# Performance work log

Measured on AMD Instinct MI355X. Metric: run time of the kernel, lower is better.

Reference implementation:

```python
import jax, jax.numpy as jnp
import numpy as np

D_MODEL = 1024
NUM_HEADS = 16
HEAD_DIM = D_MODEL // NUM_HEADS


def setup_inputs() -> dict:
    key = jax.random.key(0)
    ks = jax.random.split(key, 9)
    B, S = 2, 2048
    scale = 1.0 / np.sqrt(D_MODEL)
    inp = {
        "x": jax.random.normal(ks[0], (B, S, D_MODEL), dtype=jnp.float32),
        "Wq": jax.random.normal(ks[1], (D_MODEL, D_MODEL), dtype=jnp.float32) * scale,
        "bq": jnp.zeros((D_MODEL,), dtype=jnp.float32),
        "Wk": jax.random.normal(ks[2], (D_MODEL, D_MODEL), dtype=jnp.float32) * scale,
        "bk": jnp.zeros((D_MODEL,), dtype=jnp.float32),
        "Wv": jax.random.normal(ks[3], (D_MODEL, D_MODEL), dtype=jnp.float32) * scale,
        "bv": jnp.zeros((D_MODEL,), dtype=jnp.float32),
        "Wo": jax.random.normal(ks[4], (D_MODEL, D_MODEL), dtype=jnp.float32) * scale,
        "bo": jnpp_zeros(D_MODEL) if False else jnp.zeros((D_MODEL,), dtype=jnp.float32),
    }
    return inp


def reference(x, Wq, bq, Wk, bk, Wv, bv, Wo, bo):
    B, S, _ = x.shape
    # projections (torch Linear: y = x @ W.T + b; here W stored as [in, out])
    q = x @ Wq + bq  # [B,S,D]
    k = x @ Wk + bk
    v = x @ Wv + bv
    # split heads -> [B,H,S,hd]
    def split(t):
        return t.reshape(B, S, NUM_HEADS, HEAD_DIM).transpose(0, 2, 1, 3)
    q, k, v = split(q), split(k), split(v)
    scale = 1.0 / jnp.sqrt(jnp.asarray(HEAD_DIM, dtype=x.dtype))
    scores = jnp.einsum("bhqd,bhkd->bhqk", q, k) * scale  # [B,H,S,S]
    probs = jax.nn.softmax(scores, axis=-1)
    out = jnp.einsum("bhqk,bhkd->bhqd", probs, v)  # [B,H,S,hd]
    out = out.transpose(0, 2, 1, 3).reshape(B, S, D_MODEL)
    return out @ Wo + bo  # dropout is identity in eval mode
```

## Files before the change

kernel.cpp:

```cpp
#include <hip/hip_runtime.h>

#define D_MODEL 1024
#define NHEADS  16
#define HDIM    64
#define BATCH   2
#define SEQ     2048
#define M_TOK   (BATCH * SEQ)

typedef unsigned short u16;
typedef unsigned int   u32;
typedef __attribute__((ext_vector_type(8))) short  short8;
typedef __attribute__((ext_vector_type(4))) float  floatx4;
typedef __attribute__((ext_vector_type(2))) u32    u32x2;

#define GLOBAL_AS __attribute__((address_space(1)))
#define LDS_AS    __attribute__((address_space(3)))

static __device__ __forceinline__ void gload_lds16(const u16* g, u16* l) {
    __builtin_amdgcn_global_load_lds((const GLOBAL_AS u32*)g, (LDS_AS u32*)l, 16, 0, 0);
}

static __device__ __forceinline__ u16 f2bf(float f) {
    union { float f; u32 i; } v; v.f = f;
    u32 x = v.i;
    return (u16)((x + 0x7fffu + ((x >> 16) & 1u)) >> 16);
}

static __device__ __forceinline__ u32 cvtpk(float a, float b) {
    u32 r;
    asm("v_cvt_pk_bf16_f32 %0, %1, %2" : "=v"(r) : "v"(a), "v"(b));
    return r;
}

static __device__ __forceinline__ short8 ld8_cvt(const float* __restrict__ p) {
    float4 f0 = *(const float4*)(p);
    float4 f1 = *(const float4*)(p + 4);
    short8 r;
    r[0] = (short)f2bf(f0.x); r[1] = (short)f2bf(f0.y);
    r[2] = (short)f2bf(f0.z); r[3] = (short)f2bf(f0.w);
    r[4] = (short)f2bf(f1.x); r[5] = (short)f2bf(f1.y);
    r[6] = (short)f2bf(f1.z); r[7] = (short)f2bf(f1.w);
    return r;
}

__global__ __launch_bounds__(256) void zerofill_k(float* __restrict__ out, int n) {
    int i = blockIdx.x * 256 + threadIdx.x;
    if (i < n) out[i] = 0.f;
}

__global__ __launch_bounds__(256) void prep_k(const float* __restrict__ x,
                                              const float* __restrict__ W0,
                                              const float* __restrict__ W1,
                                              const float* __restrict__ W2,
                                              const float* __restrict__ W3,
                                              u16* __restrict__ WtBase,
                                              u16* __restrict__ Xb) {
    int z = blockIdx.z;
    int t = threadIdx.x;
    if (z == 4) {
        int blk = blockIdx.y * 32 + blockIdx.x;
        size_t i0 = ((size_t)blk * 256 + t) * 16;
        short8 v0 = ld8_cvt(x + i0);
        short8 v1 = ld8_cvt(x + i0 + 8);
        *(short8*)(Xb + i0)     = v0;
        *(short8*)(Xb + i0 + 8) = v1;
        return;
    }
    const float* W = (z == 0) ? W0 : (z == 1) ? W1 : (z == 2) ? W2 : W3;
    u16* Wt = WtBase + (size_t)z * 1024 * 1024;
    __shared__ u16 T[32][34];
    int bx = blockIdx.x * 32, by = blockIdx.y * 32;
    {
        int r = t >> 3, c4 = t & 7;
        float4 f = *(const float4*)(W + (size_t)(by + r) * 1024 + bx + c4 * 4);
        u32 lo = (u32)f2bf(f.x) | ((u32)f2bf(f.y) << 16);
        u32 hi = (u32)f2bf(f.z) | ((u32)f2bf(f.w) << 16);
        *(u32*)(&T[r][c4 * 4])     = lo;
        *(u32*)(&T[r][c4 * 4 + 2]) = hi;
    }
    __syncthreads();
    if (t < 128) {
        int n = t >> 2, seg = t & 3;
        short8 v;
#pragma unroll
        for (int i = 0; i < 8; ++i) v[i] = (short)T[seg * 8 + i][n];
        *(short8*)(Wt + (size_t)(bx + n) * 1024 + by + seg * 8) = v;
    }
}

template <int MODE, int OUTF32, int MI>
static __device__ __forceinline__ void gemm_core(u16* __restrict__ smem,
                                                 const u16* __restrict__ A,
                                                 const u16* __restrict__ Bt,
                                                 const float* __restrict__ bias,
                                                 float scale,
                                                 void* __restrict__ C,
                                                 int m0, int n0) {
    u16* As = smem;
    u16* Bs = smem + MI * 32 * 64;
    int tid  = threadIdx.x;
    int wave = tid >> 6, lane = tid & 63;
    int quad = lane >> 4, l15 = lane & 15;
    int wm = (wave & 1) * (MI * 16);
    int wn = (wave >> 1) * 64;

    floatx4 acc[MI][4] = {};

    for (int k0 = 0; k0 < 1024; k0 += 64) {
#pragma unroll
        for (int t = 0; t < MI; ++t) {
            int a = t * 256 + tid;
            int row = a >> 3, c = a & 7;
            gload_lds16(A + (size_t)(m0 + row) * 1024 + k0 + ((c ^ (row & 7)) * 8),
                        As + (size_t)a * 8);
        }
#pragma unroll
        for (int t = 0; t < 4; ++t) {
            int a = t * 256 + tid;
            int row = a >> 3, c = a & 7;
            gload_lds16(Bt + (size_t)(n0 + row) * 1024 + k0 + ((c ^ (row & 7)) * 8),
                        Bs + (size_t)a * 8);
        }
        __syncthreads();

#pragma unroll
        for (int h = 0; h < 2; ++h) {
            int g = ((h * 4 + quad) ^ (l15 & 7)) * 8;
            short8 af[MI], bfr[4];
#pragma unroll
            for (int i = 0; i < MI; ++i)
                af[i] = *(const short8*)(As + (wm + i * 16 + l15) * 64 + g);
#pragma unroll
            for (int j = 0; j < 4; ++j)
                bfr[j] = *(const short8*)(Bs + (wn + j * 16 + l15) * 64 + g);
#pragma unroll
            for (int i = 0; i < MI; ++i)
#pragma unroll
                for (int j = 0; j < 4; ++j)
                    acc[i][j] = __builtin_amdgcn_mfma_f32_16x16x32_bf16(af[i], bfr[j], acc[i][j], 0, 0, 0);
        }
        __syncthreads();
    }

    if constexpr (MODE == 2) {
        u16* T = smem;
        int bb = m0 >> 11;
#pragma unroll
        for (int p = 0; p < 2; ++p) {
            if (p) __syncthreads();
            if ((wave >> 1) == p) {
#pragma unroll
                for (int j = 0; j < 4; ++j) {
                    int dcol = j * 16 + l15;
                    float bv = bias[n0 + p * 64 + dcol];
#pragma unroll
                    for (int i = 0; i < MI; ++i) {
#pragma unroll
                        for (int rr = 0; rr < 2; ++rr) {
                            int srow = wm + i * 16 + quad * 4 + rr * 2;
                            u16 lo = f2bf((acc[i][j][rr * 2]     + bv) * scale);
                            u16 hi = f2bf((acc[i][j][rr * 2 + 1] + bv) * scale);
                            *(u32*)(T + dcol * 136 + srow) = (u32)lo | ((u32)hi << 16);
                        }
                    }
                }
            }
            __syncthreads();
            int d  = tid >> 2;
            int sc = (tid & 3) * 32;
            int col = n0 + p * 64 + d;
            int h = col >> 6, dd = col & 63;
            int s0 = (m0 & 2047) + sc;
            size_t gbase = (((size_t)bb * NHEADS + h) * HDIM + dd) * SEQ + s0;
#pragma unroll
            for (int c = 0; c < 4; ++c)
                *(short8*)((u16*)C + gbase + c * 8) = *(const short8*)(T + d * 136 + sc + c * 8);
        }
        return;
    }

#pragma unroll
    for (int j = 0; j < 4; ++j) {
        int col = n0 + wn + j * 16 + l15;
        float bv = bias[col];
#pragma unroll
        for (int i = 0; i < MI; ++i) {
#pragma unroll
            for (int r = 0; r < 4; ++r) {
                int row = m0 + wm + i * 16 + quad * 4 + r;
                float v = (acc[i][j][r] + bv) * scale;
                size_t idx;
                if (MODE == 0) {
                    idx = (size_t)row * 1024 + col;
                } else {
                    int b = row >> 11, s = row & 2047;
                    int h = col >> 6,  d = col & 63;
                    idx = (((size_t)b * NHEADS + h) * SEQ + s) * HDIM + d;
                }
                if constexpr (OUTF32) ((float*)C)[idx] = v;
                else                  ((u16*)C)[idx] = f2bf(v);
            }
        }
    }
}

__global__ __launch_bounds__(256, 3) void gemm_qkv(const u16* __restrict__ X,
                                                   const u16* __restrict__ WtBase,
                                                   const float* __restrict__ bq,
                                                   const float* __restrict__ bk,
                                                   const float* __restrict__ bv,
                                                   u16* __restrict__ OutBase) {
    __shared__ __align__(16) u16 smem[16384];
    int z = blockIdx.z;
    const u16* Bt     = WtBase + (size_t)z * 1024 * 1024;
    const float* bias = (z == 0) ? bq : (z == 1) ? bk : bv;
    u16* C            = OutBase + (size_t)z * (size_t)M_TOK * 1024;
    if (z == 2)
        gemm_core<2, 0, 4>(smem, X, Bt, bias, 1.0f, C, blockIdx.y * 128, blockIdx.x * 128);
    else if (z == 0)
        gemm_core<1, 0, 4>(smem, X, Bt, bias, 0.18033688011112042f , C,
                           blockIdx.y * 128, blockIdx.x * 128);
    else
        gemm_core<1, 0, 4>(smem, X, Bt, bias, 1.0f, C, blockIdx.y * 128, blockIdx.x * 128);
}

__global__ __launch_bounds__(256, 2) void gemm_out(const u16* __restrict__ A,
                                                   const u16* __restrict__ Bt,
                                                   const float* __restrict__ bias,
                                                   float* __restrict__ C) {
    __shared__ __align__(16) u16 smem[12288];
    gemm_core<0, 1, 2>(smem, A, Bt, bias, 1.0f, C, blockIdx.y * 64, blockIdx.x * 128);
}

#define PST2 40
__global__ __launch_bounds__(512, 3) void attn_k(const u16* __restrict__ Q,
                                                 const u16* __restrict__ K,
                                                 const u16* __restrict__ Vt_g,
                                                 u16* __restrict__ O) {
    __shared__ __align__(16) u16 Vt[2][64 * 128];
    __shared__ __align__(16) u16 Kt[2][128 * 64];
    __shared__ __align__(16) u16 Pl[8][16 * PST2];

    int tid  = threadIdx.x;
    int wave = tid >> 6, lane = tid & 63;
    int quad = lane >> 4, l15 = lane & 15;
    int bh = blockIdx.y;
    int b = bh >> 4, h = bh & 15;
    const u16* Qb = Q    + (size_t)bh * SEQ * HDIM;
    const u16* Kb = K    + (size_t)bh * SEQ * HDIM;
    const u16* Vb = Vt_g + (size_t)bh * HDIM * SEQ;
    int q0 = blockIdx.x * 128 + wave * 16;

    short8 qf0 = *(const short8*)(Qb + (size_t)(q0 + l15) * 64 + quad * 8);
    short8 qf1 = *(const short8*)(Qb + (size_t)(q0 + l15) * 64 + 32 + quad * 8);

    short8 onesf;
#pragma unroll
    for (int i = 0; i < 8; ++i) onesf[i] = (short)0x3F80;

    floatx4 o[4] = {};
    floatx4 o_sum = {};

    {
#pragma unroll
        for (int rnd = 0; rnd < 2; ++rnd) {
            int g = rnd * 512 + tid;
            int vrow = g >> 4, vc = g & 15;
            gload_lds16(Vb + (size_t)vrow * SEQ + (vc ^ (vrow & 15)) * 8,
                        Vt[0] + (size_t)g * 8);
            int krow = g >> 3, kc = g & 7;
            gload_lds16(Kb + (size_t)krow * 64 + (kc ^ (krow & 7)) * 8,
                        Kt[0] + (size_t)g * 8);
        }
    }

    for (int it = 0; it < SEQ / 128; ++it) {
        int kv0 = it * 128;
        __syncthreads();

        if (it + 1 < SEQ / 128) {
            u16* vdst = Vt[(it + 1) & 1];
            u16* kdst = Kt[(it + 1) & 1];
#pragma unroll
            for (int rnd = 0; rnd < 2; ++rnd) {
                int g = rnd * 512 + tid;
                int vrow = g >> 4, vc = g & 15;
                gload_lds16(Vb + (size_t)vrow * SEQ + kv0 + 128 + (vc ^ (vrow & 15)) * 8,
                            vdst + (size_t)g * 8);
                int krow = g >> 3, kc = g & 7;
                gload_lds16(Kb + (size_t)(kv0 + 128 + krow) * 64 + (kc ^ (krow & 7)) * 8,
                            kdst + (size_t)g * 8);
            }
        }

        const u16* kb = Kt[it & 1];
        floatx4 s[8];
        __builtin_amdgcn_s_setprio(1);
#pragma unroll
        for (int j = 0; j < 8; ++j) {
            int row = j * 16 + l15;
            const u16* kr = kb + (size_t)row * 64;
            short8 k0 = *(const short8*)(kr + ((quad ^ (l15 & 7)) * 8));
            short8 k1 = *(const short8*)(kr + (((quad + 4) ^ (l15 & 7)) * 8));
            floatx4 a = {};
            a = __builtin_amdgcn_mfma_f32_16x16x32_bf16(k0, qf0, a, 0, 0, 0);
            a = __builtin_amdgcn_mfma_f32_16x16x32_bf16(k1, qf1, a, 0, 0, 0);
            s[j] = a;
        }
        __builtin_amdgcn_s_setprio(0);

        const u16* vb = Vt[it & 1];
#pragma unroll
        for (int kh = 0; kh < 4; ++kh) {
#pragma unroll
            for (int t = 0; t < 2; ++t) {
                int j = kh * 2 + t;
                float p0 = exp2f(s[j][0]), p1 = exp2f(s[j][1]);
                float p2 = exp2f(s[j][2]), p3 = exp2f(s[j][3]);
                u32 w0 = cvtpk(p0, p1), w1 = cvtpk(p2, p3);
                *(u32x2*)(&Pl[wave][l15 * PST2 + t * 16 + quad * 4]) = (u32x2){w0, w1};
            }
            short8 pf = *(const short8*)(&Pl[wave][l15 * PST2 + quad * 8]);
            __builtin_amdgcn_s_setprio(1);
#pragma unroll
            for (int dj = 0; dj < 4; ++dj) {
                int row = dj * 16 + l15;
                int cg  = kh * 4 + quad;
                short8 vf = *(const short8*)(&vb[(row * 16 + (cg ^ l15)) * 8]);
                o[dj] = __builtin_amdgcn_mfma_f32_16x16x32_bf16(pf, vf, o[dj], 0, 0, 0);
            }
            o_sum = __builtin_amdgcn_mfma_f32_16x16x32_bf16(pf, onesf, o_sum, 0, 0, 0);
            __builtin_amdgcn_s_setprio(0);
        }
    }

#pragma unroll
    for (int r = 0; r < 4; ++r) {
        float invq = 1.f / o_sum[r];
        int srow = q0 + quad * 4 + r;
        size_t base = ((size_t)b * SEQ + srow) * D_MODEL + h * HDIM;
#pragma unroll
        for (int dj = 0; dj < 4; ++dj)
            O[base + dj * 16 + l15] = f2bf(o[dj][r] * invq);
    }
}

extern "C" void kernel_launch(void* const* d_in, const int* in_sizes, int n_in,
                              void* d_out, int out_size, void* d_ws, size_t ws_size,
                              hipStream_t stream) {
    const float* x  = (const float*)d_in[0];
    const float* Wq = (const float*)d_in[1];
    const float* bq = (const float*)d_in[2];
    const float* Wk = (const float*)d_in[3];
    const float* bk = (const float*)d_in[4];
    const float* Wv = (const float*)d_in[5];
    const float* bv = (const float*)d_in[6];
    const float* Wo = (const float*)d_in[7];
    const float* bo = (const float*)d_in[8];
    float* out = (float*)d_out;

    char* ws = (char*)d_ws;
    const size_t WSZ = (size_t)1024 * 1024 * sizeof(u16);
    const size_t QSZ = (size_t)M_TOK * 1024 * sizeof(u16);
    const size_t NEED = 4 * WSZ + 4 * QSZ;

    if (ws_size < NEED) {
        zerofill_k<<<dim3((out_size + 255) / 256), 256, 0, stream>>>(out, out_size);
        return;
    }

    u16* wtq = (u16*)(ws);
    u16* wto = (u16*)(ws + 3 * WSZ);
    u16* Qw  = (u16*)(ws + 4 * WSZ);
    u16* Kw  = (u16*)(ws + 4 * WSZ + QSZ);
    u16* Vw  = (u16*)(ws + 4 * WSZ + 2 * QSZ);
    u16* Xb  = (u16*)(ws + 4 * WSZ + 3 * QSZ);
    u16* Aw  = Xb;

    prep_k<<<dim3(32, 32, 5), 256, 0, stream>>>(x, Wq, Wk, Wv, Wo, wtq, Xb);

    gemm_qkv<<<dim3(8, 32, 3), 256, 0, stream>>>(Xb, wtq, bq, bk, bv, Qw);
    attn_k<<<dim3(SEQ / 128, BATCH * NHEADS), 512, 0, stream>>>(Qw, Kw, Vw, Aw);
    gemm_out<<<dim3(8, 64), 256, 0, stream>>>(Aw, wto, bo, out);
}
```

Baseline: 196.6 us.

## Double-buffer GEMM K-loop with async LDS prefetch and per-kernel BK

Adds a templated K-tile size and double-buffers the GEMM main loop. The next tile is now issued via global_load_lds before the current tile's MFMAs run, so there is one barrier per iteration instead of two. The QKV GEMM switches to BK=32 tiles with no XOR swizzle so the double buffer fits its existing shared-memory size. The output GEMM keeps BK=64 and doubles its shared allocation. This is meant to hide global load latency behind compute, at the cost of possible LDS bank conflicts in the unswizzled BK=32 layout and more shared memory in gemm_out.

```diff
diff --git a/kernel.cpp b/kernel.cpp
--- a/kernel.cpp
+++ b/kernel.cpp
@@ -88,7 +88,7 @@
     }
 }
 
-template <int MODE, int OUTF32, int MI>
+template <int MODE, int OUTF32, int MI, int BK>
 static __device__ __forceinline__ void gemm_core(u16* __restrict__ smem,
                                                  const u16* __restrict__ A,
                                                  const u16* __restrict__ Bt,
@@ -96,53 +96,70 @@
                                                  float scale,
                                                  void* __restrict__ C,
                                                  int m0, int n0) {
-    u16* As = smem;
-    u16* Bs = smem + MI * 32 * 64;
+    constexpr int RG   = BK / 8;
+    constexpr int BUFG = (MI * 32 + 128) * RG;
     int tid  = threadIdx.x;
     int wave = tid >> 6, lane = tid & 63;
     int quad = lane >> 4, l15 = lane & 15;
     int wm = (wave & 1) * (MI * 16);
     int wn = (wave >> 1) * 64;
 
+    auto stage = [&](int buf, int k0) {
+        u16* Asb = smem + (size_t)buf * BUFG * 8;
+        u16* Bsb = Asb + MI * 32 * RG * 8;
+#pragma unroll
+        for (int t = 0; t < MI * 32 * RG / 256; ++t) {
+            int a = t * 256 + tid;
+            int row = a / RG, c = a & (RG - 1);
+            int cs = (BK == 64) ? (c ^ (row & 7)) : c;
+            gload_lds16(A + (size_t)(m0 + row) * 1024 + k0 + cs * 8,
+                        Asb + (size_t)a * 8);
+        }
+#pragma unroll
+        for (int t = 0; t < 128 * RG / 256; ++t) {
+            int a = t * 256 + tid;
+            int row = a / RG, c = a & (RG - 1);
+            int cs = (BK == 64) ? (c ^ (row & 7)) : c;
+            gload_lds16(Bt + (size_t)(n0 + row) * 1024 + k0 + cs * 8,
+                        Bsb + (size_t)a * 8);
+        }
+    };
+
     floatx4 acc[MI][4] = {};
-
-    for (int k0 = 0; k0 < 1024; k0 += 64) {
-#pragma unroll
-        for (int t = 0; t < MI; ++t) {
-            int a = t * 256 + tid;
-            int row = a >> 3, c = a & 7;
-            gload_lds16(A + (size_t)(m0 + row) * 1024 + k0 + ((c ^ (row & 7)) * 8),
-                        As + (size_t)a * 8);
-        }
-#pragma unroll
-        for (int t = 0; t < 4; ++t) {
-            int a = t * 256 + tid;
-            int row = a >> 3, c = a & 7;
-            gload_lds16(Bt + (size_t)(n0 + row) * 1024 + k0 + ((c ^ (row & 7)) * 8),
-                        Bs + (size_t)a * 8);
-        }
+    stage(0, 0);
+
+    for (int k0 = 0; k0 < 1024; k0 += BK) {
+        int cur = (k0 / BK) & 1;
         __syncthreads();
-
-#pragma unroll
-        for (int h = 0; h < 2; ++h) {
-            int g = ((h * 4 + quad) ^ (l15 & 7)) * 8;
+        if (k0 + BK < 1024) stage(cur ^ 1, k0 + BK);
+
+        u16* Asb = smem + (size_t)cur * BUFG * 8;
+        u16* Bsb = Asb + MI * 32 * RG * 8;
+#pragma unroll
+        for (int h = 0; h < BK / 32; ++h) {
             short8 af[MI], bfr[4];
 #pragma unroll
-            for (int i = 0; i < MI; ++i)
-                af[i] = *(const short8*)(As + (wm + i * 16 + l15) * 64 + g);
-#pragma unroll
-            for (int j = 0; j < 4; ++j)
-                bfr[j] = *(const short8*)(Bs + (wn + j * 16 + l15) * 64 + g);
+            for (int i = 0; i < MI; ++i) {
+                int row = wm + i * 16 + l15;
+                int g = (BK == 64) ? ((h * 4 + quad) ^ (l15 & 7)) : quad;
+                af[i] = *(const short8*)(Asb + (size_t)row * BK + g * 8);
+            }
+#pragma unroll
+            for (int j = 0; j < 4; ++j) {
+                int row = wn + j * 16 + l15;
+                int g = (BK == 64) ? ((h * 4 + quad) ^ (l15 & 7)) : quad;
+                bfr[j] = *(const short8*)(Bsb + (size_t)row * BK + g * 8);
+            }
 #pragma unroll
             for (int i = 0; i < MI; ++i)
 #pragma unroll
                 for (int j = 0; j < 4; ++j)
                     acc[i][j] = __builtin_amdgcn_mfma_f32_16x16x32_bf16(af[i], bfr[j], acc[i][j], 0, 0, 0);
         }
+    }
+
+    if constexpr (MODE == 2) {
         __syncthreads();
-    }
-
-    if constexpr (MODE == 2) {
         u16* T = smem;
         int bb = m0 >> 11;
 #pragma unroll
@@ -216,20 +233,20 @@
     const float* bias = (z == 0) ? bq : (z == 1) ? bk : bv;
     u16* C            = OutBase + (size_t)z * (size_t)M_TOK * 1024;
     if (z == 2)
-        gemm_core<2, 0, 4>(smem, X, Bt, bias, 1.0f, C, blockIdx.y * 128, blockIdx.x * 128);
+        gemm_core<2, 0, 4, 32>(smem, X, Bt, bias, 1.0f, C, blockIdx.y * 128, blockIdx.x * 128);
     else if (z == 0)
-        gemm_core<1, 0, 4>(smem, X, Bt, bias, 0.18033688011112042f , C,
-                           blockIdx.y * 128, blockIdx.x * 128);
+        gemm_core<1, 0, 4, 32>(smem, X, Bt, bias, 0.18033688011112042f , C,
+                               blockIdx.y * 128, blockIdx.x * 128);
     else
-        gemm_core<1, 0, 4>(smem, X, Bt, bias, 1.0f, C, blockIdx.y * 128, blockIdx.x * 128);
+        gemm_core<1, 0, 4, 32>(smem, X, Bt, bias, 1.0f, C, blockIdx.y * 128, blockIdx.x * 128);
 }
 
 __global__ __launch_bounds__(256, 2) void gemm_out(const u16* __restrict__ A,
                                                    const u16* __restrict__ Bt,
                                                    const float* __restrict__ bias,
                                                    float* __restrict__ C) {
-    __shared__ __align__(16) u16 smem[12288];
-    gemm_core<0, 1, 2>(smem, A, Bt, bias, 1.0f, C, blockIdx.y * 64, blockIdx.x * 128);
+    __shared__ __align__(16) u16 smem[24576];
+    gemm_core<0, 1, 2, 64>(smem, A, Bt, bias, 1.0f, C, blockIdx.y * 64, blockIdx.x * 128);
 }
 
 #define PST2 40
```

Measured after the change: 196.2 us. No clear change (-0.2%).

## Triple-buffer GEMM K-loop with async LDS loads and XCD-aware block remap

Applied to the files above, without the earlier changes.

Restructures the shared GEMM core so the K loop runs in 32-wide steps over three LDS buffers. Loads for step k+2 are issued before the MFMAs of step k, and explicit vmcnt waits plus a single barrier per step replace the two syncthreads per 64-wide step. It also drops the XOR swizzle, which may reintroduce LDS bank conflicts. The QKV and output GEMM grids remap block indices so that consecutive logical tiles land on the same XCD for L2 reuse. Larger LDS use may lower occupancy.

```diff
diff --git a/kernel.cpp b/kernel.cpp
--- a/kernel.cpp
+++ b/kernel.cpp
@@ -96,53 +96,64 @@
                                                  float scale,
                                                  void* __restrict__ C,
                                                  int m0, int n0) {
-    u16* As = smem;
-    u16* Bs = smem + MI * 32 * 64;
+    constexpr int BUFU = (MI * 32 + 128) * 32;
+    constexpr int NK   = 32;
     int tid  = threadIdx.x;
     int wave = tid >> 6, lane = tid & 63;
     int quad = lane >> 4, l15 = lane & 15;
     int wm = (wave & 1) * (MI * 16);
     int wn = (wave >> 1) * 64;
 
+    auto stage = [&](int buf, int k0) {
+        u16* Asb = smem + (size_t)buf * BUFU;
+        u16* Bsb = Asb + MI * 32 * 32;
+#pragma unroll
+        for (int t = 0; t < MI / 2; ++t) {
+            int a = t * 256 + tid;
+            gload_lds16(A + (size_t)(m0 + (a >> 2)) * 1024 + k0 + (a & 3) * 8,
+                        Asb + (size_t)a * 8);
+        }
+#pragma unroll
+        for (int t = 0; t < 2; ++t) {
+            int a = t * 256 + tid;
+            gload_lds16(Bt + (size_t)(n0 + (a >> 2)) * 1024 + k0 + (a & 3) * 8,
+                        Bsb + (size_t)a * 8);
+        }
+    };
+
     floatx4 acc[MI][4] = {};
-
-    for (int k0 = 0; k0 < 1024; k0 += 64) {
-#pragma unroll
-        for (int t = 0; t < MI; ++t) {
-            int a = t * 256 + tid;
-            int row = a >> 3, c = a & 7;
-            gload_lds16(A + (size_t)(m0 + row) * 1024 + k0 + ((c ^ (row & 7)) * 8),
-                        As + (size_t)a * 8);
-        }
-#pragma unroll
-        for (int t = 0; t < 4; ++t) {
-            int a = t * 256 + tid;
-            int row = a >> 3, c = a & 7;
-            gload_lds16(Bt + (size_t)(n0 + row) * 1024 + k0 + ((c ^ (row & 7)) * 8),
-                        Bs + (size_t)a * 8);
-        }
+    stage(0, 0);
+    stage(1, 32);
+
+    for (int k = 0; k < NK; ++k) {
+        if (k + 1 < NK) {
+            if constexpr (MI == 4) asm volatile("s_waitcnt vmcnt(4)" ::: "memory");
+            else                   asm volatile("s_waitcnt vmcnt(3)" ::: "memory");
+        } else {
+            asm volatile("s_waitcnt vmcnt(0)" ::: "memory");
+        }
+        __builtin_amdgcn_s_barrier();
+        __builtin_amdgcn_sched_barrier(0);
+        if (k + 2 < NK) stage((k + 2) % 3, (k + 2) * 32);
+
+        u16* Asb = smem + (size_t)(k % 3) * BUFU;
+        u16* Bsb = Asb + MI * 32 * 32;
+        short8 af[MI], bfr[4];
+#pragma unroll
+        for (int i = 0; i < MI; ++i)
+            af[i] = *(const short8*)(Asb + (wm + i * 16 + l15) * 32 + quad * 8);
+#pragma unroll
+        for (int j = 0; j < 4; ++j)
+            bfr[j] = *(const short8*)(Bsb + (wn + j * 16 + l15) * 32 + quad * 8);
+#pragma unroll
+        for (int i = 0; i < MI; ++i)
+#pragma unroll
+            for (int j = 0; j < 4; ++j)
+                acc[i][j] = __builtin_amdgcn_mfma_f32_16x16x32_bf16(af[i], bfr[j], acc[i][j], 0, 0, 0);
+    }
+
+    if constexpr (MODE == 2) {
         __syncthreads();
-
-#pragma unroll
-        for (int h = 0; h < 2; ++h) {
-            int g = ((h * 4 + quad) ^ (l15 & 7)) * 8;
-            short8 af[MI], bfr[4];
-#pragma unroll
-            for (int i = 0; i < MI; ++i)
-                af[i] = *(const short8*)(As + (wm + i * 16 + l15) * 64 + g);
-#pragma unroll
-            for (int j = 0; j < 4; ++j)
-                bfr[j] = *(const short8*)(Bs + (wn + j * 16 + l15) * 64 + g);
-#pragma unroll
-            for (int i = 0; i < MI; ++i)
-#pragma unroll
-                for (int j = 0; j < 4; ++j)
-                    acc[i][j] = __builtin_amdgcn_mfma_f32_16x16x32_bf16(af[i], bfr[j], acc[i][j], 0, 0, 0);
-        }
-        __syncthreads();
-    }
-
-    if constexpr (MODE == 2) {
         u16* T = smem;
         int bb = m0 >> 11;
 #pragma unroll
@@ -210,26 +221,32 @@
                                                    const float* __restrict__ bk,
                                                    const float* __restrict__ bv,
                                                    u16* __restrict__ OutBase) {
-    __shared__ __align__(16) u16 smem[16384];
-    int z = blockIdx.z;
+    __shared__ __align__(16) u16 smem[24576];
+    int hw = blockIdx.z * 256 + blockIdx.y * 8 + blockIdx.x;
+    int lg = (hw & 7) * 96 + (hw >> 3);
+    int z  = lg >> 8;
+    int rem = lg & 255;
+    int m0 = (rem >> 3) * 128, n0 = (rem & 7) * 128;
     const u16* Bt     = WtBase + (size_t)z * 1024 * 1024;
     const float* bias = (z == 0) ? bq : (z == 1) ? bk : bv;
     u16* C            = OutBase + (size_t)z * (size_t)M_TOK * 1024;
     if (z == 2)
-        gemm_core<2, 0, 4>(smem, X, Bt, bias, 1.0f, C, blockIdx.y * 128, blockIdx.x * 128);
+        gemm_core<2, 0, 4>(smem, X, Bt, bias, 1.0f, C, m0, n0);
     else if (z == 0)
-        gemm_core<1, 0, 4>(smem, X, Bt, bias, 0.18033688011112042f , C,
-                           blockIdx.y * 128, blockIdx.x * 128);
+        gemm_core<1, 0, 4>(smem, X, Bt, bias, 0.18033688011112042f , C, m0, n0);
     else
-        gemm_core<1, 0, 4>(smem, X, Bt, bias, 1.0f, C, blockIdx.y * 128, blockIdx.x * 128);
+        gemm_core<1, 0, 4>(smem, X, Bt, bias, 1.0f, C, m0, n0);
 }
 
 __global__ __launch_bounds__(256, 2) void gemm_out(const u16* __restrict__ A,
                                                    const u16* __restrict__ Bt,
                                                    const float* __restrict__ bias,
                                                    float* __restrict__ C) {
-    __shared__ __align__(16) u16 smem[12288];
-    gemm_core<0, 1, 2>(smem, A, Bt, bias, 1.0f, C, blockIdx.y * 64, blockIdx.x * 128);
+    __shared__ __align__(16) u16 smem[18432];
+    int hw = blockIdx.y * 8 + blockIdx.x;
+    int lg = (hw & 7) * 64 + (hw >> 3);
+    int m0 = (lg >> 3) * 64, n0 = (lg & 7) * 128;
+    gemm_core<0, 1, 2>(smem, A, Bt, bias, 1.0f, C, m0, n0);
 }
 
 #define PST2 40
```

Result: slower. 202.9 us (+3.2%).
